# Optimization experiments

Hardware: AMD Instinct MI355X
Metric: run time of the kernel (lower is better)

The kernel has to match this reference:

```python
import jax, jax.numpy as jnp
import numpy as np

NEG = -1e30  # effective -inf in fp32 log-space
BLANK = 0


def _rnnt_forward(pred_pad, target, pred_len, target_len):
    """RNNT loss (warp-rnnt semantics, gather=True, reduction='mean').

    pred_pad: [B, T, U+1, V] joint logits; target: [B, U] labels;
    pred_len, target_len: [B] valid lengths.
    """
    log_probs = jax.nn.log_softmax(pred_pad.astype(jnp.float32), axis=-1)
    B, T, U1, V = log_probs.shape
    U = U1 - 1
    blank_lp = log_probs[..., BLANK]                       # [B, T, U+1]
    # label emission log-prob at (t, u): P(target[u] | t, u), only for u < U
    label_lp = jnp.take_along_axis(
        log_probs[:, :, :U, :], target[:, None, :, None].astype(jnp.int32), axis=-1
    )[..., 0]                                              # [B, T, U]
    label_lp = jnp.pad(label_lp, ((0, 0), (0, 0), (0, 1)), constant_values=NEG)  # [B,T,U+1]

    def per_seq(blank, label):  # blank, label: [T, U+1]
        # alpha[0, u] = sum_{u'<u} label[0, u']
        row0 = jnp.concatenate([jnp.zeros((1,), jnp.float32),
                                jnp.cumsum(label[0, :-1])])

        def comb(x, y):
            a1, b1 = x
            a2, b2 = y
            return (a1 + a2, jnp.logaddexp(b2, b1 + a2))

        def step(prev_row, inp):
            blank_prev, label_t = inp            # blank[t-1], label[t]
            base = prev_row + blank_prev         # vertical (blank) transition
            # horizontal recurrence: row[u] = logaddexp(base[u], row[u-1] + label_t[u-1])
            a = jnp.concatenate([jnp.full((1,), NEG, jnp.float32), label_t[:-1]])
            _, row = jax.lax.associative_scan(comb, (a, base))
            return row, row

        _, rows = jax.lax.scan(step, row0, (blank[:-1], label[1:]))
        return jnp.concatenate([row0[None, :], rows], axis=0)  # [T, U+1]

    alphas = jax.vmap(per_seq)(blank_lp, label_lp)            # [B, T, U+1]
    b_idx = jnp.arange(B)
    t_idx = pred_len.astype(jnp.int32) - 1
    u_idx = target_len.astype(jnp.int32)
    ll = alphas[b_idx, t_idx, u_idx] + blank_lp[b_idx, t_idx, u_idx]
    return -jnp.mean(ll)


def setup_inputs() -> dict:
    key = jax.random.key(0)
    k1, k2, k3, k4 = jax.random.split(key, 4)
    B, T, U, V = 8, 128, 64, 1024
    pred_pad = jax.random.normal(k1, (B, T, U + 1, V), dtype=jnp.float32)
    target = jax.random.randint(k2, (B, U), 1, V, dtype=jnp.int32)  # avoid blank=0
    pred_len = jax.random.randint(k3, (B,), T // 2, T + 1, dtype=jnp.int32)
    target_len = jax.random.randint(k4, (B,), U // 2, U + 1, dtype=jnp.int32)
    return {"pred_pad": pred_pad, "target": target,
            "pred_len": pred_len, "target_len": target_len}


def reference(pred_pad, target, pred_len, target_len):
    return _rnnt_forward(pred_pad, target, pred_len, target_len)
```

## Files before the change

### kernel.cpp

```cpp
#include <hip/hip_runtime.h>

#define NEGF   (-1e30f)
#define T_DIM  128
#define U_DIM  64
#define U1     65
#define V_DIM  1024
#define B_DIM  8
#define DMAX   192
#define L2E    1.4426950408889634f
#define LN2    0.6931471805599453f

__device__ __forceinline__ float fexp2(float x) {
    float r; asm("v_exp_f32 %0, %1" : "=v"(r) : "v"(x)); return r;
}
__device__ __forceinline__ float flog2(float x) {
    float r; asm("v_log_f32 %0, %1" : "=v"(r) : "v"(x)); return r;
}

__global__ __launch_bounds__(256) void lse_kernel(
    const float* __restrict__ pred, const int* __restrict__ target,
    const int* __restrict__ pred_len, const int* __restrict__ target_len,
    float* __restrict__ pairF, float* __restrict__ out)
{
    if (blockIdx.x == 0 && threadIdx.x == 0) out[0] = 0.0f;

    const int wave = blockIdx.x * 4 + (threadIdx.x >> 6);
    const int lane = threadIdx.x & 63;
    const int b   = wave / (T_DIM * U1);
    const int rem = wave - b * (T_DIM * U1);
    const int t   = rem / U1;
    const int u   = rem - t * U1;

    if (t >= pred_len[b] || u > target_len[b]) return;

    const float*  row = pred + (size_t)wave * V_DIM;
    const float4* r4  = (const float4*)row;

    float4 a0 = r4[lane];
    float4 a1 = r4[lane + 64];
    float4 a2 = r4[lane + 128];
    float4 a3 = r4[lane + 192];

    float s = __expf(a0.x) + __expf(a0.y) + __expf(a0.z) + __expf(a0.w)
            + __expf(a1.x) + __expf(a1.y) + __expf(a1.z) + __expf(a1.w)
            + __expf(a2.x) + __expf(a2.y) + __expf(a2.z) + __expf(a2.w)
            + __expf(a3.x) + __expf(a3.y) + __expf(a3.z) + __expf(a3.w);
    #pragma unroll
    for (int off = 32; off; off >>= 1) s += __shfl_xor(s, off);

    const float l2s = flog2(s);

    if (lane == 0) {
        const int base = (b * DMAX + t + u) * U1;
        pairF[2 * (base + u)] = a0.x * L2E - l2s;
        if (u < U_DIM) {
            const int tg = target[b * U_DIM + u];
            pairF[2 * (base + u + 1) + 1] = row[tg] * L2E - l2s;
        }
    }
}

template<bool W64>
__device__ __forceinline__ float alpha_body(
    const float2* smem, const int u, const int d_end, const int uq)
{
    float cur = (u == 0) ? 0.0f : NEGF;
    float a64 = NEGF;

#define SLOT_DECL(K) float bl##K, lam##K, bl64##K, l63##K;
    SLOT_DECL(0) SLOT_DECL(1) SLOT_DECL(2) SLOT_DECL(3)
    SLOT_DECL(4) SLOT_DECL(5) SLOT_DECL(6) SLOT_DECL(7)

#define LOAD_SLOT(K, r) { \
        int rr = (r); if (rr > d_end) rr = d_end; \
        float2 a = smem[rr * U1 + u]; \
        bl##K  = (u <= rr) ? a.x : NEGF; \
        lam##K = ((unsigned)(u - 1) <= (unsigned)rr) ? a.y : NEGF; \
        if (W64) { \
            float2 qq = smem[rr * U1 + U_DIM]; \
            bl64##K = (rr >= U_DIM) ? qq.x : NEGF; \
            l63##K  = (rr >= 63)    ? qq.y : NEGF; \
        } else { bl64##K = NEGF; l63##K = NEGF; } \
    }

#define STEP(K) { \
        float h_pre = __int_as_float(__builtin_amdgcn_update_dpp( \
            0, __float_as_int(cur), 0x138 , 0xf, 0xf, true)); \
        float a63_ = W64 ? __int_as_float( \
            __builtin_amdgcn_readlane(__float_as_int(cur), 63)) : 0.0f; \
        float v = cur + bl##K; \
        float h = h_pre + lam##K; \
        float m = fmaxf(v, h); \
        cur = m + flog2(1.0f + fexp2(-fabsf(v - h))); \
        if (W64) { \
            float v2 = a64 + bl64##K; \
            float h2 = a63_ + l63##K; \
            float m2 = fmaxf(v2, h2); \
            a64 = m2 + flog2(1.0f + fexp2(-fabsf(v2 - h2))); \
        } \
    }

    LOAD_SLOT(0, 0) LOAD_SLOT(1, 1) LOAD_SLOT(2, 2) LOAD_SLOT(3, 3)
    LOAD_SLOT(4, 4) LOAD_SLOT(5, 5) LOAD_SLOT(6, 6) LOAD_SLOT(7, 7)

    int db = 1;
    for (; db + 7 <= d_end; db += 8) {
        STEP(0) LOAD_SLOT(0, db + 7)
        STEP(1) LOAD_SLOT(1, db + 8)
        STEP(2) LOAD_SLOT(2, db + 9)
        STEP(3) LOAD_SLOT(3, db + 10)
        STEP(4) LOAD_SLOT(4, db + 11)
        STEP(5) LOAD_SLOT(5, db + 12)
        STEP(6) LOAD_SLOT(6, db + 13)
        STEP(7) LOAD_SLOT(7, db + 14)
    }
    if (db + 0 <= d_end) STEP(0)
    if (db + 1 <= d_end) STEP(1)
    if (db + 2 <= d_end) STEP(2)
    if (db + 3 <= d_end) STEP(3)
    if (db + 4 <= d_end) STEP(4)
    if (db + 5 <= d_end) STEP(5)
    if (db + 6 <= d_end) STEP(6)

#undef STEP
#undef LOAD_SLOT
#undef SLOT_DECL

    float val = W64 ? a64 : __shfl(cur, uq);
    float fb  = smem[d_end * U1 + uq].x;
    return (val + fb) * LN2;
}

__global__ __launch_bounds__(64) void alpha_kernel(
    const float* __restrict__ pairF,
    const int* __restrict__ pred_len, const int* __restrict__ target_len,
    float* __restrict__ out)
{
    __shared__ __align__(16) float2 smem[DMAX * U1 + 64];

    const int b  = blockIdx.x;
    const int u  = threadIdx.x;
    const int tl = pred_len[b];
    const int uq = target_len[b];
    const int d_end = tl - 1 + uq;

    const float* srcF = pairF + (size_t)b * (2 * DMAX * U1);

    const int niter = ((d_end + 1) * U1 + 127) >> 7;
    for (int i = 0; i < niter; ++i) {
        const float* g = srcF + (size_t)i * 256 + u * 4;
        __builtin_amdgcn_global_load_lds(
            (const __attribute__((address_space(1))) void*)g,
            (__attribute__((address_space(3))) void*)(&smem[i * 128]),
            16, 0, 0);
    }
    asm volatile("s_waitcnt vmcnt(0)" ::: "memory");

    float ll = (uq == U_DIM) ? alpha_body<true >(smem, u, d_end, uq)
                             : alpha_body<false>(smem, u, d_end, uq);

    if (u == 0) atomicAdd(out, -ll * (1.0f / B_DIM));
}

extern "C" void kernel_launch(void* const* d_in, const int* in_sizes, int n_in,
                              void* d_out, int out_size, void* d_ws, size_t ws_size,
                              hipStream_t stream) {
    const float* pred       = (const float*)d_in[0];
    const int*   target     = (const int*)d_in[1];
    const int*   pred_len   = (const int*)d_in[2];
    const int*   target_len = (const int*)d_in[3];
    float* out = (float*)d_out;

    float* pairF = (float*)d_ws;

    const int nrows = B_DIM * T_DIM * U1;
    lse_kernel<<<nrows / 4, 256, 0, stream>>>(pred, target, pred_len, target_len,
                                              pairF, out);
    alpha_kernel<<<B_DIM, 64, 0, stream>>>(pairF, pred_len, target_len, out);
}
```

Measured before the change: 39.24 us.

## Fuse log-softmax producer and alpha recurrence into one kernel with per-diagonal flags

Merges the two kernels into a single launch. The first 8 blocks act as consumers that run the alpha recurrence per batch and spin on per-anti-diagonal completion counters. The remaining blocks produce the blank and label log-probs and bump those counters, so the recurrence can start before all rows are reduced. Producers now interleave the batch index so that early diagonals are produced first for all sequences. They also read the label logit from registers via a shuffle instead of re-reading global memory, and use nontemporal loads. This adds a memset launch and cross-block spin-waiting, which relies on consumer blocks being resident and on memory ordering at agent scope.

```diff
diff --git a/kernel.cpp b/kernel.cpp
--- a/kernel.cpp
+++ b/kernel.cpp
@@ -10,6 +10,11 @@
 #define L2E    1.4426950408889634f
 #define LN2    0.6931471805599453f
 
+#define FLAGS_OFF  8
+#define PAIR_OFF_F 2048
+
+typedef float f32x4 __attribute__((ext_vector_type(4)));
+
 __device__ __forceinline__ float fexp2(float x) {
     float r; asm("v_exp_f32 %0, %1" : "=v"(r) : "v"(x)); return r;
 }
@@ -17,29 +22,39 @@
     float r; asm("v_log_f32 %0, %1" : "=v"(r) : "v"(x)); return r;
 }
 
-__global__ __launch_bounds__(256) void lse_kernel(
+__device__ __forceinline__ int ld_flag(const int* p) {
+    return __hip_atomic_load((int*)p, __ATOMIC_RELAXED, __HIP_MEMORY_SCOPE_AGENT);
+}
+__device__ __forceinline__ float2 ld_f2c(const float2* p) {
+    union { unsigned long long u; float2 f; } c;
+    c.u = __hip_atomic_load((unsigned long long*)p, __ATOMIC_RELAXED,
+                            __HIP_MEMORY_SCOPE_AGENT);
+    return c.f;
+}
+__device__ __forceinline__ void st_fc(float* p, float v) {
+    __hip_atomic_store(p, v, __ATOMIC_RELAXED, __HIP_MEMORY_SCOPE_AGENT);
+}
+
+__device__ __forceinline__ void produce(
+    int wave, int lane,
     const float* __restrict__ pred, const int* __restrict__ target,
     const int* __restrict__ pred_len, const int* __restrict__ target_len,
-    float* __restrict__ pairF, float* __restrict__ out)
-{
-    if (blockIdx.x == 0 && threadIdx.x == 0) out[0] = 0.0f;
-
-    const int wave = blockIdx.x * 4 + (threadIdx.x >> 6);
-    const int lane = threadIdx.x & 63;
-    const int b   = wave / (T_DIM * U1);
-    const int rem = wave - b * (T_DIM * U1);
-    const int t   = rem / U1;
-    const int u   = rem - t * U1;
+    float* __restrict__ pairF, int* __restrict__ flags)
+{
+    const int b    = wave & 7;
+    const int rest = wave >> 3;
+    const int t    = rest / U1;
+    const int u    = rest - t * U1;
 
     if (t >= pred_len[b] || u > target_len[b]) return;
 
-    const float*  row = pred + (size_t)wave * V_DIM;
-    const float4* r4  = (const float4*)row;
-
-    float4 a0 = r4[lane];
-    float4 a1 = r4[lane + 64];
-    float4 a2 = r4[lane + 128];
-    float4 a3 = r4[lane + 192];
+    const size_t rw = (size_t)(b * T_DIM + t) * U1 + u;
+    const f32x4* r4 = (const f32x4*)(pred + rw * V_DIM);
+
+    f32x4 a0 = __builtin_nontemporal_load(r4 + lane);
+    f32x4 a1 = __builtin_nontemporal_load(r4 + lane + 64);
+    f32x4 a2 = __builtin_nontemporal_load(r4 + lane + 128);
+    f32x4 a3 = __builtin_nontemporal_load(r4 + lane + 192);
 
     float s = __expf(a0.x) + __expf(a0.y) + __expf(a0.z) + __expf(a0.w)
             + __expf(a1.x) + __expf(a1.y) + __expf(a1.z) + __expf(a1.w)
@@ -47,119 +62,157 @@
             + __expf(a3.x) + __expf(a3.y) + __expf(a3.z) + __expf(a3.w);
     #pragma unroll
     for (int off = 32; off; off >>= 1) s += __shfl_xor(s, off);
-
     const float l2s = flog2(s);
 
+    float labv = 0.0f;
+    if (u < U_DIM) {
+        const int tg = target[b * U_DIM + u];
+        const int g = tg >> 8, c = tg & 3, sl = (tg >> 2) & 63;
+        f32x4 ag   = (g == 0) ? a0 : (g == 1) ? a1 : (g == 2) ? a2 : a3;
+        float  cmp = (c == 0) ? ag.x : (c == 1) ? ag.y : (c == 2) ? ag.z : ag.w;
+        labv = __shfl(cmp, sl);
+    }
+
+    const int d = t + u;
     if (lane == 0) {
-        const int base = (b * DMAX + t + u) * U1;
-        pairF[2 * (base + u)] = a0.x * L2E - l2s;
-        if (u < U_DIM) {
-            const int tg = target[b * U_DIM + u];
-            pairF[2 * (base + u + 1) + 1] = row[tg] * L2E - l2s;
-        }
+        float* base = pairF + 2 * (size_t)((b * DMAX + d) * U1);
+        st_fc(base + 2 * u, a0.x * L2E - l2s);
+        if (u < U_DIM) st_fc(base + 2 * (u + 1) + 1, labv * L2E - l2s);
+        asm volatile("s_waitcnt vmcnt(0)" ::: "memory");
+        __hip_atomic_fetch_add(&flags[b * DMAX + d], 1,
+                               __ATOMIC_RELAXED, __HIP_MEMORY_SCOPE_AGENT);
+    }
+}
+
+__device__ __forceinline__ void poll8(const int* __restrict__ flg, int r0,
+                                      int d_end, int tl, int uq, int lane)
+{
+    const int r = r0 + lane;
+    const bool need = (lane < 8) && (r <= d_end);
+    int expect = 0;
+    if (need) {
+        int lo = r - tl + 1; if (lo < 0) lo = 0;
+        int hi = (r < uq) ? r : uq;
+        expect = hi - lo + 1;
+    }
+    const int* fp = flg + (need ? r : 0);
+    for (;;) {
+        int have = need ? ld_flag(fp) : 0;
+        if (__all(have >= expect)) return;
     }
 }
 
 template<bool W64>
-__device__ __forceinline__ float alpha_body(
-    const float2* smem, const int u, const int d_end, const int uq)
+__device__ __forceinline__ float consume(
+    const float2* __restrict__ pr,
+    const int* __restrict__ flg,
+    const int u, const int d_end, const int tl, const int uq)
 {
     float cur = (u == 0) ? 0.0f : NEGF;
     float a64 = NEGF;
 
-#define SLOT_DECL(K) float bl##K, lam##K, bl64##K, l63##K;
-    SLOT_DECL(0) SLOT_DECL(1) SLOT_DECL(2) SLOT_DECL(3)
-    SLOT_DECL(4) SLOT_DECL(5) SLOT_DECL(6) SLOT_DECL(7)
-
-#define LOAD_SLOT(K, r) { \
-        int rr = (r); if (rr > d_end) rr = d_end; \
-        float2 a = smem[rr * U1 + u]; \
-        bl##K  = (u <= rr) ? a.x : NEGF; \
-        lam##K = ((unsigned)(u - 1) <= (unsigned)rr) ? a.y : NEGF; \
-        if (W64) { \
-            float2 qq = smem[rr * U1 + U_DIM]; \
-            bl64##K = (rr >= U_DIM) ? qq.x : NEGF; \
-            l63##K  = (rr >= 63)    ? qq.y : NEGF; \
-        } else { bl64##K = NEGF; l63##K = NEGF; } \
-    }
-
-#define STEP(K) { \
+    float2 raw0, raw1, raw2, raw3, raw4, raw5, raw6, raw7;
+    float2 q0, q1, q2, q3, q4, q5, q6, q7;
+
+#define LOADS(K, r) { \
+        int rr_ = (r); if (rr_ > d_end) rr_ = d_end; \
+        raw##K = ld_f2c(pr + rr_ * U1 + u); \
+        if (W64) q##K = ld_f2c(pr + rr_ * U1 + U_DIM); }
+
+#define STEP(K, RI) { \
+        const int rr_ = (RI); \
         float h_pre = __int_as_float(__builtin_amdgcn_update_dpp( \
             0, __float_as_int(cur), 0x138 , 0xf, 0xf, true)); \
         float a63_ = W64 ? __int_as_float( \
             __builtin_amdgcn_readlane(__float_as_int(cur), 63)) : 0.0f; \
-        float v = cur + bl##K; \
-        float h = h_pre + lam##K; \
+        float bl  = (u <= rr_) ? raw##K.x : NEGF; \
+        float lam = ((unsigned)(u - 1) <= (unsigned)rr_) ? raw##K.y : NEGF; \
+        float v = cur + bl; \
+        float h = h_pre + lam; \
         float m = fmaxf(v, h); \
         cur = m + flog2(1.0f + fexp2(-fabsf(v - h))); \
         if (W64) { \
-            float v2 = a64 + bl64##K; \
-            float h2 = a63_ + l63##K; \
+            float bl64 = (rr_ >= U_DIM) ? q##K.x : NEGF; \
+            float l63  = (rr_ >= 63)    ? q##K.y : NEGF; \
+            float v2 = a64 + bl64; \
+            float h2 = a63_ + l63; \
             float m2 = fmaxf(v2, h2); \
-            a64 = m2 + flog2(1.0f + fexp2(-fabsf(v2 - h2))); \
-        } \
-    }
-
-    LOAD_SLOT(0, 0) LOAD_SLOT(1, 1) LOAD_SLOT(2, 2) LOAD_SLOT(3, 3)
-    LOAD_SLOT(4, 4) LOAD_SLOT(5, 5) LOAD_SLOT(6, 6) LOAD_SLOT(7, 7)
+            a64 = m2 + flog2(1.0f + fexp2(-fabsf(v2 - h2))); } }
+
+    poll8(flg, 0, d_end, tl, uq, u);
+    LOADS(0, 0) LOADS(1, 1) LOADS(2, 2) LOADS(3, 3)
+    LOADS(4, 4) LOADS(5, 5) LOADS(6, 6) LOADS(7, 7)
 
     int db = 1;
     for (; db + 7 <= d_end; db += 8) {
-        STEP(0) LOAD_SLOT(0, db + 7)
-        STEP(1) LOAD_SLOT(1, db + 8)
-        STEP(2) LOAD_SLOT(2, db + 9)
-        STEP(3) LOAD_SLOT(3, db + 10)
-        STEP(4) LOAD_SLOT(4, db + 11)
-        STEP(5) LOAD_SLOT(5, db + 12)
-        STEP(6) LOAD_SLOT(6, db + 13)
-        STEP(7) LOAD_SLOT(7, db + 14)
-    }
-    if (db + 0 <= d_end) STEP(0)
-    if (db + 1 <= d_end) STEP(1)
-    if (db + 2 <= d_end) STEP(2)
-    if (db + 3 <= d_end) STEP(3)
-    if (db + 4 <= d_end) STEP(4)
-    if (db + 5 <= d_end) STEP(5)
-    if (db + 6 <= d_end) STEP(6)
+        poll8(flg, db + 7, d_end, tl, uq, u);
+        STEP(0, db - 1)  LOADS(0, db + 7)
+        STEP(1, db    )  LOADS(1, db + 8)
+        STEP(2, db + 1)  LOADS(2, db + 9)
+        STEP(3, db + 2)  LOADS(3, db + 10)
+        STEP(4, db + 3)  LOADS(4, db + 11)
+        STEP(5, db + 4)  LOADS(5, db + 12)
+        STEP(6, db + 5)  LOADS(6, db + 13)
+        STEP(7, db + 6)  LOADS(7, db + 14)
+    }
+    if (db + 0 <= d_end) STEP(0, db - 1)
+    if (db + 1 <= d_end) STEP(1, db    )
+    if (db + 2 <= d_end) STEP(2, db + 1)
+    if (db + 3 <= d_end) STEP(3, db + 2)
+    if (db + 4 <= d_end) STEP(4, db + 3)
+    if (db + 5 <= d_end) STEP(5, db + 4)
+    if (db + 6 <= d_end) STEP(6, db + 5)
 
 #undef STEP
-#undef LOAD_SLOT
-#undef SLOT_DECL
+#undef LOADS
 
     float val = W64 ? a64 : __shfl(cur, uq);
-    float fb  = smem[d_end * U1 + uq].x;
+    float fb  = ld_f2c(pr + d_end * U1 + uq).x;
     return (val + fb) * LN2;
 }
 
-__global__ __launch_bounds__(64) void alpha_kernel(
-    const float* __restrict__ pairF,
+__global__ __launch_bounds__(256) void rnnt_fused(
+    const float* __restrict__ pred, const int* __restrict__ target,
     const int* __restrict__ pred_len, const int* __restrict__ target_len,
-    float* __restrict__ out)
-{
-    __shared__ __align__(16) float2 smem[DMAX * U1 + 64];
-
-    const int b  = blockIdx.x;
-    const int u  = threadIdx.x;
-    const int tl = pred_len[b];
-    const int uq = target_len[b];
-    const int d_end = tl - 1 + uq;
-
-    const float* srcF = pairF + (size_t)b * (2 * DMAX * U1);
-
-    const int niter = ((d_end + 1) * U1 + 127) >> 7;
-    for (int i = 0; i < niter; ++i) {
-        const float* g = srcF + (size_t)i * 256 + u * 4;
-        __builtin_amdgcn_global_load_lds(
-            (const __attribute__((address_space(1))) void*)g,
-            (__attribute__((address_space(3))) void*)(&smem[i * 128]),
-            16, 0, 0);
-    }
-    asm volatile("s_waitcnt vmcnt(0)" ::: "memory");
-
-    float ll = (uq == U_DIM) ? alpha_body<true >(smem, u, d_end, uq)
-                             : alpha_body<false>(smem, u, d_end, uq);
-
-    if (u == 0) atomicAdd(out, -ll * (1.0f / B_DIM));
+    float* __restrict__ ws, float* __restrict__ out)
+{
+    float* acc   = ws;
+    int*   done  = (int*)ws + 1;
+    int*   flags = (int*)ws + FLAGS_OFF;
+    float* pairF = ws + PAIR_OFF_F;
+
+    const int tid  = threadIdx.x;
+    const int lane = tid & 63;
+    const int widx = tid >> 6;
+
+    if (blockIdx.x < B_DIM) {
+        if (widx != 0) return;
+        const int b  = blockIdx.x;
+        const int tl = pred_len[b];
+        const int uq = target_len[b];
+        const int d_end = tl - 1 + uq;
+        const float2* pr = (const float2*)pairF + (size_t)b * DMAX * U1;
+        const int* flg = flags + b * DMAX;
+
+        float ll = (uq == U_DIM) ? consume<true >(pr, flg, lane, d_end, tl, uq)
+                                 : consume<false>(pr, flg, lane, d_end, tl, uq);
+
+        if (lane == 0) {
+            atomicAdd(acc, -ll * (1.0f / B_DIM));
+            asm volatile("s_waitcnt vmcnt(0)" ::: "memory");
+            int prev = __hip_atomic_fetch_add(done, 1, __ATOMIC_RELAXED,
+                                              __HIP_MEMORY_SCOPE_AGENT);
+            if (prev == B_DIM - 1) {
+                float r = __hip_atomic_load(acc, __ATOMIC_RELAXED,
+                                            __HIP_MEMORY_SCOPE_AGENT);
+                out[0] = r;
+            }
+        }
+        return;
+    }
+
+    const int wave = (blockIdx.x - B_DIM) * 4 + widx;
+    produce(wave, lane, pred, target, pred_len, target_len, pairF, flags);
 }
 
 extern "C" void kernel_launch(void* const* d_in, const int* in_sizes, int n_in,
@@ -170,11 +223,13 @@
     const int*   pred_len   = (const int*)d_in[2];
     const int*   target_len = (const int*)d_in[3];
     float* out = (float*)d_out;
-
-    float* pairF = (float*)d_ws;
-
-    const int nrows = B_DIM * T_DIM * U1;
-    lse_kernel<<<nrows / 4, 256, 0, stream>>>(pred, target, pred_len, target_len,
-                                              pairF, out);
-    alpha_kernel<<<B_DIM, 64, 0, stream>>>(pairF, pred_len, target_len, out);
-}
+    float* ws  = (float*)d_ws;
+
+    (void)hipMemsetAsync(d_ws, 0,
+                         (size_t)(FLAGS_OFF + B_DIM * DMAX) * sizeof(int),
+                         stream);
+
+    const int nprod = (B_DIM * T_DIM * U1) / 4;
+    rnnt_fused<<<B_DIM + nprod, 256, 0, stream>>>(pred, target, pred_len,
+                                                  target_len, ws, out);
+}
```

Measured after the change: 50.10 us. 1.28x slower.
